# Optimization experiments

Hardware: AMD Instinct MI355X
Metric: run time of the kernel (lower is better)

## Reference

```python
import jax, jax.numpy as jnp
import numpy as np

C, H, W = 512, 192, 192  # feature map dims; 3x3 patches at stride 3 (non-overlapping)


def setup_inputs() -> dict:
    key = jax.random.key(0)
    k1, k2 = jax.random.split(key)
    model_resp = jax.random.normal(k1, (1, C, H, W), dtype=jnp.float32)
    style_resp = jax.random.normal(k2, (1, C, H, W), dtype=jnp.float32)
    return {"model_resp": model_resp, "style_resp": style_resp}


def _unfold3(x):
    # torch.nn.Unfold(kernel=3, stride=3) on (1, C, H, W) -> (C*9, L) after the
    # module's view(patch_count, patch_size) (note: rows are feature channels,
    # columns are spatial locations, matching the original code's dim order).
    _, c, h, w = x.shape
    p = x[0].reshape(c, h // 3, 3, w // 3, 3)          # (c, ph, kh, pw, kw)
    p = p.transpose(0, 2, 4, 1, 3)                      # (c, kh, kw, ph, pw)
    return p.reshape(c * 9, (h // 3) * (w // 3))        # (A, L)


def reference(model_resp, style_resp):
    img = _unfold3(model_resp)                          # (A, L)
    sty = _unfold3(style_resp)                          # (A, L)
    img_norm = 1.0 / jnp.linalg.norm(img, axis=1)       # (A,)
    sty_norm = 1.0 / jnp.linalg.norm(sty, axis=1)       # (A,)
    S = img @ sty.T                                     # (A, A), S[i,j] = img_i . sty_j
    # Faithful to torch: expand(A, A) of a 1-D tensor broadcasts along dim 0,
    # i.e. multiplies COLUMNS by the normalizer vector.
    S1 = S * img_norm[None, :]
    S2 = S1.T * sty_norm[None, :]                       # S2[i,j] = img_norm[i]*sty_norm[j]*(img_j . sty_i)
    nearest = jnp.argmax(S2, axis=0)                    # (A,) int
    max_sim = jnp.max(S2, axis=0)                       # (A,) float (the online-max values)
    return nearest, max_sim
```

## Files before the change

kernel.cpp:

```cpp
#include <hip/hip_runtime.h>
#include <hip/hip_bf16.h>
#include <hip/hip_fp16.h>

#define A_DIM 4608
#define L_DIM 4096
#define CH    512
#define H_DIM 192
#define W_DIM 192

#define BM 128
#define BN 192
#define BK 16
#define NS (L_DIM / BK)

#define CPB 32

typedef _Float16 half8 __attribute__((ext_vector_type(8)));
typedef float   floatx4 __attribute__((ext_vector_type(4)));
typedef float   floatx16 __attribute__((ext_vector_type(16)));

__global__ __launch_bounds__(256) void prep_kernel(
    const float* __restrict__ x0, const float* __restrict__ x1,
    _Float16* __restrict__ Uhi0, _Float16* __restrict__ Ulo0,
    _Float16* __restrict__ Uhi1, _Float16* __restrict__ Ulo1,
    float* __restrict__ ss0, float* __restrict__ ss1) {
  const int which = blockIdx.z;
  const float* __restrict__ x = which ? x1 : x0;
  _Float16* __restrict__ Uhi = which ? Uhi1 : Uhi0;
  _Float16* __restrict__ Ulo = which ? Ulo1 : Ulo0;
  float* __restrict__ ssg = which ? ss1 : ss0;

  const int ph = blockIdx.y;
  const int c0 = blockIdx.x * CPB;
  const int abase = blockIdx.x * (CPB * 9);

  __shared__ _Float16 sHi[CPB * 9 * 8 * 8];
  __shared__ _Float16 sLo[CPB * 9 * 8 * 8];

  const int t = threadIdx.x;

  const int c_l = t >> 3;
  const int s = t & 7;
  const float* __restrict__ rowbase =
      x + ((size_t)(c0 + c_l) * H_DIM + 3 * ph) * W_DIM + s * 24;
  float ssp[9] = {0.f, 0.f, 0.f, 0.f, 0.f, 0.f, 0.f, 0.f, 0.f};

#pragma unroll
  for (int kh = 0; kh < 3; ++kh) {
    const float* __restrict__ rp = rowbase + kh * W_DIM;
    floatx4 v4[6];
#pragma unroll
    for (int i = 0; i < 6; ++i) v4[i] = *(const floatx4*)(rp + i * 4);
    half8 hv[3], lv[3];
#pragma unroll
    for (int i = 0; i < 6; ++i)
#pragma unroll
      for (int j = 0; j < 4; ++j) {
        const int m = i * 4 + j;
        const int kw = m % 3, e = m / 3;
        const float v = v4[i][j];
        ssp[kh * 3 + kw] += v * v;
        const _Float16 h = (_Float16)v;
        hv[kw][e] = h;
        lv[kw][e] = (_Float16)(v - (float)h);
      }
#pragma unroll
    for (int kw = 0; kw < 3; ++kw) {
      const int a_l = c_l * 9 + kh * 3 + kw;
      const int addr = (a_l * 8 + (s ^ (a_l & 7))) * 8;
      *(half8*)&sHi[addr] = hv[kw];
      *(half8*)&sLo[addr] = lv[kw];
    }
  }
#pragma unroll
  for (int q = 0; q < 9; ++q) {
    float v = ssp[q];
    v += __shfl_down(v, 4, 8);
    v += __shfl_down(v, 2, 8);
    v += __shfl_down(v, 1, 8);
    if (s == 0) atomicAdd(&ssg[abase + c_l * 9 + q], v);
  }
  __syncthreads();

#pragma unroll
  for (int i = 0; i < 9; ++i) {
    const int idx = i * 256 + t;
    const int c8 = idx / 288;
    const int a_l = idx - c8 * 288;
    const int addr = (a_l * 8 + (c8 ^ (a_l & 7))) * 8;
    const size_t g = ((size_t)(ph * 8 + c8) * A_DIM + abase + a_l) * 8;
    *(half8*)&Uhi[g] = *(const half8*)&sHi[addr];
    *(half8*)&Ulo[g] = *(const half8*)&sLo[addr];
  }
}

#define GLDS(g, l)                                                          \
  __builtin_amdgcn_global_load_lds(                                        \
      (const __attribute__((address_space(1))) void*)(g),                   \
      (__attribute__((address_space(3))) void*)(l), 16, 0, 0)

#define MFMA_(A, B, C) __builtin_amdgcn_mfma_f32_32x32x16_f16(A, B, C, 0, 0, 0)

__global__ __launch_bounds__(256, 2) void gemm_max_kernel(
    const _Float16* __restrict__ Shi, const _Float16* __restrict__ Slo,
    const _Float16* __restrict__ Ihi, const _Float16* __restrict__ Ilo,
    const float* __restrict__ img_ss,
    unsigned long long* __restrict__ packed) {
  __shared__ _Float16 sm[3 * 10240];

  const int t = threadIdx.x;
  const int lane = t & 63, wv = t >> 6;
  const int wvr = wv >> 1, wvc = wv & 1;
  const int id = blockIdx.x;
  const int g = id / 288, r = id - g * 288;
  const int by = r >> 3, bx = g * 8 + (r & 7);
  const int row0 = by * BM;
  const int col0 = bx * BN;
  const int l31 = lane & 31, hs = lane >> 5;

  floatx16 acc[2][3];
#pragma unroll
  for (int rf = 0; rf < 2; ++rf)
#pragma unroll
    for (int cf = 0; cf < 3; ++cf) acc[rf][cf] = (floatx16)0.f;

  const size_t CH8 = (size_t)A_DIM * 8;

  const size_t aOff = (size_t)(t >> 7) * CH8 + (size_t)(row0 + (t & 127)) * 8;
  const int aDst = t * 8;
  const size_t bG0 =
      (size_t)(t / 192) * CH8 + (size_t)(col0 + (t % 192)) * 8;
  const int bD0 = 4096 + t * 8;
  const int c1 = 256 + t;
  const int mat1 = (c1 >= 384) ? 1 : 0;
  const int rem1 = c1 - mat1 * 384;
  const _Float16* __restrict__ bP1 = mat1 ? Ilo : Ihi;
  const size_t bG1 =
      (size_t)(rem1 / 192) * CH8 + (size_t)(col0 + (rem1 % 192)) * 8;
  const int bD1 = 4096 + mat1 * 3072 + rem1 * 8;
  const int rem2 = 128 + t;
  const size_t bG2 =
      (size_t)(rem2 / 192) * CH8 + (size_t)(col0 + (rem2 % 192)) * 8;
  const int bD2 = 7168 + rem2 * 8;

#define ISSUE(BB, koff)                                  \
  do {                                                   \
    GLDS(Shi + (koff) + aOff, &sm[(BB) + aDst]);         \
    GLDS(Slo + (koff) + aOff, &sm[(BB) + 2048 + aDst]);  \
    GLDS(Ihi + (koff) + bG0, &sm[(BB) + bD0]);           \
    GLDS(bP1 + (koff) + bG1, &sm[(BB) + bD1]);           \
    GLDS(Ilo + (koff) + bG2, &sm[(BB) + bD2]);           \
  } while (0)

  const int aI = (hs * 128 + wvr * 64 + l31) * 8;
  const int bI = (hs * 192 + wvc * 96 + l31) * 8;

  ISSUE(0, 0);
  ISSUE(10240, 2 * CH8);

  int bufC = 0, bufP = 20480;
  for (int ks = 0; ks < NS; ++ks) {
    if (ks < NS - 1) {
      asm volatile("s_waitcnt vmcnt(5)" ::: "memory");
    } else {
      asm volatile("s_waitcnt vmcnt(0)" ::: "memory");
    }
    asm volatile("s_barrier" ::: "memory");

    if (ks + 2 < NS) ISSUE(bufP, (size_t)(ks + 2) * 2 * CH8);

    half8 ah[2], al[2], bh[3], bl[3];
#pragma unroll
    for (int rf = 0; rf < 2; ++rf) {
      ah[rf] = *(const half8*)&sm[bufC + aI + rf * 256];
      al[rf] = *(const half8*)&sm[bufC + 2048 + aI + rf * 256];
    }
#pragma unroll
    for (int cf = 0; cf < 3; ++cf) {
      bh[cf] = *(const half8*)&sm[bufC + 4096 + bI + cf * 256];
      bl[cf] = *(const half8*)&sm[bufC + 7168 + bI + cf * 256];
    }
#pragma unroll
    for (int rf = 0; rf < 2; ++rf)
#pragma unroll
      for (int cf = 0; cf < 3; ++cf)
        acc[rf][cf] = MFMA_(ah[rf], bh[cf], acc[rf][cf]);
#pragma unroll
    for (int rf = 0; rf < 2; ++rf)
#pragma unroll
      for (int cf = 0; cf < 3; ++cf)
        acc[rf][cf] = MFMA_(ah[rf], bl[cf], acc[rf][cf]);
#pragma unroll
    for (int rf = 0; rf < 2; ++rf)
#pragma unroll
      for (int cf = 0; cf < 3; ++cf)
        acc[rf][cf] = MFMA_(al[rf], bh[cf], acc[rf][cf]);

    bufC = (bufC == 20480) ? 0 : bufC + 10240;
    bufP = (bufP == 20480) ? 0 : bufP + 10240;
  }

  float nrv[2][16];
#pragma unroll
  for (int rf = 0; rf < 2; ++rf) {
    const int base_i = row0 + wvr * 64 + rf * 32 + 4 * hs;
#pragma unroll
    for (int g2 = 0; g2 < 4; ++g2) {
      const floatx4 s4 = *(const floatx4*)&img_ss[base_i + 8 * g2];
#pragma unroll
      for (int r2 = 0; r2 < 4; ++r2) nrv[rf][g2 * 4 + r2] = 1.0f / sqrtf(s4[r2]);
    }
  }
#pragma unroll
  for (int cf = 0; cf < 3; ++cf) {
    const int j = col0 + wvc * 96 + cf * 32 + l31;
    float best = -3.4e38f;
    int bi = 0x7FFFFFFF;
#pragma unroll
    for (int rf = 0; rf < 2; ++rf) {
      const int base_i = row0 + wvr * 64 + rf * 32 + 4 * hs;
#pragma unroll
      for (int g2 = 0; g2 < 4; ++g2)
#pragma unroll
        for (int r2 = 0; r2 < 4; ++r2) {
          const int i = base_i + 8 * g2 + r2;
          const float v = acc[rf][cf][g2 * 4 + r2] * nrv[rf][g2 * 4 + r2];
          if (v > best) { best = v; bi = i; }
        }
    }
    const float ov = __shfl_xor(best, 32, 64);
    const int oi = __shfl_xor(bi, 32, 64);
    if (ov > best || (ov == best && oi < bi)) { best = ov; bi = oi; }
    if (hs == 0) {
      const unsigned u = __float_as_uint(best);
      const unsigned key = (u & 0x80000000u) ? ~u : (u | 0x80000000u);
      const unsigned long long pk =
          ((unsigned long long)key << 32) | (unsigned)(~(unsigned)bi);
      atomicMax(&packed[j], pk);
    }
  }
}

__global__ __launch_bounds__(256) void finalize_kernel(
    const unsigned long long* __restrict__ packed,
    const float* __restrict__ sty_ss, float* __restrict__ out) {
  const int j = blockIdx.x * 256 + threadIdx.x;
  if (j >= A_DIM) return;
  const unsigned long long p = packed[j];
  const unsigned key = (unsigned)(p >> 32);
  const unsigned u = (key & 0x80000000u) ? (key ^ 0x80000000u) : ~key;
  const float v = __uint_as_float(u);
  const int idx = (int)(~(unsigned)(p & 0xFFFFFFFFu));
  out[j] = (float)idx;
  out[A_DIM + j] = v * (1.0f / sqrtf(sty_ss[j]));
}

extern "C" void kernel_launch(void* const* d_in, const int* in_sizes, int n_in,
                              void* d_out, int out_size, void* d_ws, size_t ws_size,
                              hipStream_t stream) {
  const float* model = (const float*)d_in[0];
  const float* style = (const float*)d_in[1];
  float* out = (float*)d_out;
  char* ws = (char*)d_ws;

  const size_t usz = (size_t)A_DIM * L_DIM * 2;
  _Float16* img_hi = (_Float16*)(ws);
  _Float16* img_lo = (_Float16*)(ws + usz);
  _Float16* sty_hi = (_Float16*)(ws + 2 * usz);
  _Float16* sty_lo = (_Float16*)(ws + 3 * usz);
  float* img_ss = (float*)(ws + 4 * usz);
  float* sty_ss = img_ss + A_DIM;
  unsigned long long* packed = (unsigned long long*)(img_ss + 2 * A_DIM);

  hipMemsetAsync(img_ss, 0, (size_t)A_DIM * 16, stream);
  prep_kernel<<<dim3(CH / CPB, H_DIM / 3, 2), 256, 0, stream>>>(
      model, style, img_hi, img_lo, sty_hi, sty_lo, img_ss, sty_ss);
  gemm_max_kernel<<<dim3((A_DIM / BM) * (A_DIM / BN)), 256, 0, stream>>>(
      sty_hi, sty_lo, img_hi, img_lo, img_ss, packed);
  finalize_kernel<<<18, 256, 0, stream>>>(packed, sty_ss, out);
}
```

Baseline: 676.6 us.

## Give each wave private LDS buffers to remove block-wide barriers in GEMM loop

```diff
diff --git a/kernel.cpp b/kernel.cpp
--- a/kernel.cpp
+++ b/kernel.cpp
@@ -106,7 +106,7 @@
     const _Float16* __restrict__ Ihi, const _Float16* __restrict__ Ilo,
     const float* __restrict__ img_ss,
     unsigned long long* __restrict__ packed) {
-  __shared__ _Float16 sm[3 * 10240];
+  __shared__ _Float16 sm[4 * 2 * 5120];
 
   const int t = threadIdx.x;
   const int lane = t & 63, wv = t >> 6;
@@ -117,6 +117,7 @@
   const int row0 = by * BM;
   const int col0 = bx * BN;
   const int l31 = lane & 31, hs = lane >> 5;
+  const int wb = wv * 10240;
 
   floatx16 acc[2][3];
 #pragma unroll
@@ -126,78 +127,76 @@
 
   const size_t CH8 = (size_t)A_DIM * 8;
 
-  const size_t aOff = (size_t)(t >> 7) * CH8 + (size_t)(row0 + (t & 127)) * 8;
-  const int aDst = t * 8;
-  const size_t bG0 =
-      (size_t)(t / 192) * CH8 + (size_t)(col0 + (t % 192)) * 8;
-  const int bD0 = 4096 + t * 8;
-  const int c1 = 256 + t;
-  const int mat1 = (c1 >= 384) ? 1 : 0;
-  const int rem1 = c1 - mat1 * 384;
-  const _Float16* __restrict__ bP1 = mat1 ? Ilo : Ihi;
-  const size_t bG1 =
-      (size_t)(rem1 / 192) * CH8 + (size_t)(col0 + (rem1 % 192)) * 8;
-  const int bD1 = 4096 + mat1 * 3072 + rem1 * 8;
-  const int rem2 = 128 + t;
-  const size_t bG2 =
-      (size_t)(rem2 / 192) * CH8 + (size_t)(col0 + (rem2 % 192)) * 8;
-  const int bD2 = 7168 + rem2 * 8;
-
-#define ISSUE(BB, koff)                                  \
-  do {                                                   \
-    GLDS(Shi + (koff) + aOff, &sm[(BB) + aDst]);         \
-    GLDS(Slo + (koff) + aOff, &sm[(BB) + 2048 + aDst]);  \
-    GLDS(Ihi + (koff) + bG0, &sm[(BB) + bD0]);           \
-    GLDS(bP1 + (koff) + bG1, &sm[(BB) + bD1]);           \
-    GLDS(Ilo + (koff) + bG2, &sm[(BB) + bD2]);           \
+  const int rA = row0 + wvr * 64;
+  const int rB = col0 + wvc * 96;
+  const size_t gA0 = (size_t)(rA + lane) * 8;
+  const size_t gA1 = CH8 + gA0;
+  const size_t gB0 = (size_t)(rB + lane) * 8;
+  const size_t gB1 = (lane < 32)
+                         ? (size_t)(rB + 64 + lane) * 8
+                         : CH8 + (size_t)(rB + lane - 32) * 8;
+  const size_t gB2 = CH8 + (size_t)(rB + 32 + lane) * 8;
+  const int dl8 = lane * 8;
+
+#define ISSUE(bb, koff)                                        \
+  do {                                                         \
+    GLDS(Shi + (koff) + gA0, &sm[wb + (bb) + dl8]);            \
+    GLDS(Shi + (koff) + gA1, &sm[wb + (bb) + 512 + dl8]);      \
+    GLDS(Slo + (koff) + gA0, &sm[wb + (bb) + 1024 + dl8]);     \
+    GLDS(Slo + (koff) + gA1, &sm[wb + (bb) + 1536 + dl8]);     \
+    GLDS(Ihi + (koff) + gB0, &sm[wb + (bb) + 2048 + dl8]);     \
+    GLDS(Ihi + (koff) + gB1, &sm[wb + (bb) + 2560 + dl8]);     \
+    GLDS(Ihi + (koff) + gB2, &sm[wb + (bb) + 3072 + dl8]);     \
+    GLDS(Ilo + (koff) + gB0, &sm[wb + (bb) + 3584 + dl8]);     \
+    GLDS(Ilo + (koff) + gB1, &sm[wb + (bb) + 4096 + dl8]);     \
+    GLDS(Ilo + (koff) + gB2, &sm[wb + (bb) + 4608 + dl8]);     \
   } while (0)
 
-  const int aI = (hs * 128 + wvr * 64 + l31) * 8;
-  const int bI = (hs * 192 + wvc * 96 + l31) * 8;
+  const int aI = hs * 512 + l31 * 8;
+  const int bI = hs * 768 + l31 * 8;
+
+#define KSTEP(BOFF, KS)                                                  \
+  do {                                                                   \
+    asm volatile("s_waitcnt lgkmcnt(0)" ::: "memory");                   \
+    if ((KS) + 1 < NS) {                                                 \
+      ISSUE(5120 - (BOFF), (size_t)((KS) + 1) * 2 * CH8);                \
+      asm volatile("s_waitcnt vmcnt(10)" ::: "memory");                  \
+    } else {                                                             \
+      asm volatile("s_waitcnt vmcnt(0)" ::: "memory");                   \
+    }                                                                    \
+    const int base = wb + (BOFF);                                        \
+    half8 ah[2], al[2], bh[3], bl[3];                                    \
+    _Pragma("unroll")                                                    \
+    for (int rf = 0; rf < 2; ++rf) {                                     \
+      ah[rf] = *(const half8*)&sm[base + aI + rf * 256];                 \
+      al[rf] = *(const half8*)&sm[base + 1024 + aI + rf * 256];          \
+    }                                                                    \
+    _Pragma("unroll")                                                    \
+    for (int cf = 0; cf < 3; ++cf) {                                     \
+      bh[cf] = *(const half8*)&sm[base + 2048 + bI + cf * 256];          \
+      bl[cf] = *(const half8*)&sm[base + 3584 + bI + cf * 256];          \
+    }                                                                    \
+    _Pragma("unroll")                                                    \
+    for (int rf = 0; rf < 2; ++rf)                                       \
+      _Pragma("unroll")                                                  \
+      for (int cf = 0; cf < 3; ++cf)                                     \
+        acc[rf][cf] = MFMA_(ah[rf], bh[cf], acc[rf][cf]);                \
+    _Pragma("unroll")                                                    \
+    for (int rf = 0; rf < 2; ++rf)                                       \
+      _Pragma("unroll")                                                  \
+      for (int cf = 0; cf < 3; ++cf)                                     \
+        acc[rf][cf] = MFMA_(ah[rf], bl[cf], acc[rf][cf]);                \
+    _Pragma("unroll")                                                    \
+    for (int rf = 0; rf < 2; ++rf)                                       \
+      _Pragma("unroll")                                                  \
+      for (int cf = 0; cf < 3; ++cf)                                     \
+        acc[rf][cf] = MFMA_(al[rf], bh[cf], acc[rf][cf]);                \
+  } while (0)
 
   ISSUE(0, 0);
-  ISSUE(10240, 2 * CH8);
-
-  int bufC = 0, bufP = 20480;
-  for (int ks = 0; ks < NS; ++ks) {
-    if (ks < NS - 1) {
-      asm volatile("s_waitcnt vmcnt(5)" ::: "memory");
-    } else {
-      asm volatile("s_waitcnt vmcnt(0)" ::: "memory");
-    }
-    asm volatile("s_barrier" ::: "memory");
-
-    if (ks + 2 < NS) ISSUE(bufP, (size_t)(ks + 2) * 2 * CH8);
-
-    half8 ah[2], al[2], bh[3], bl[3];
-#pragma unroll
-    for (int rf = 0; rf < 2; ++rf) {
-      ah[rf] = *(const half8*)&sm[bufC + aI + rf * 256];
-      al[rf] = *(const half8*)&sm[bufC + 2048 + aI + rf * 256];
-    }
-#pragma unroll
-    for (int cf = 0; cf < 3; ++cf) {
-      bh[cf] = *(const half8*)&sm[bufC + 4096 + bI + cf * 256];
-      bl[cf] = *(const half8*)&sm[bufC + 7168 + bI + cf * 256];
-    }
-#pragma unroll
-    for (int rf = 0; rf < 2; ++rf)
-#pragma unroll
-      for (int cf = 0; cf < 3; ++cf)
-        acc[rf][cf] = MFMA_(ah[rf], bh[cf], acc[rf][cf]);
-#pragma unroll
-    for (int rf = 0; rf < 2; ++rf)
-#pragma unroll
-      for (int cf = 0; cf < 3; ++cf)
-        acc[rf][cf] = MFMA_(ah[rf], bl[cf], acc[rf][cf]);
-#pragma unroll
-    for (int rf = 0; rf < 2; ++rf)
-#pragma unroll
-      for (int cf = 0; cf < 3; ++cf)
-        acc[rf][cf] = MFMA_(al[rf], bh[cf], acc[rf][cf]);
-
-    bufC = (bufC == 20480) ? 0 : bufC + 10240;
-    bufP = (bufP == 20480) ? 0 : bufP + 10240;
+  for (int ks = 0; ks < NS; ks += 2) {
+    KSTEP(0, ks);
+    KSTEP(5120, ks + 1);
   }
 
   float nrv[2][16];
```

Measured after the change: 793.8 us. +17.3%, slower.

## Double-buffer LDS with register ping-pong fragments to overlap LDS reads with MFMA

Applied to the files above, without the earlier changes.

```diff
diff --git a/kernel.cpp b/kernel.cpp
--- a/kernel.cpp
+++ b/kernel.cpp
@@ -106,7 +106,7 @@
     const _Float16* __restrict__ Ihi, const _Float16* __restrict__ Ilo,
     const float* __restrict__ img_ss,
     unsigned long long* __restrict__ packed) {
-  __shared__ _Float16 sm[3 * 10240];
+  __shared__ _Float16 sm[2 * 10240];
 
   const int t = threadIdx.x;
   const int lane = t & 63, wv = t >> 6;
@@ -128,8 +128,7 @@
 
   const size_t aOff = (size_t)(t >> 7) * CH8 + (size_t)(row0 + (t & 127)) * 8;
   const int aDst = t * 8;
-  const size_t bG0 =
-      (size_t)(t / 192) * CH8 + (size_t)(col0 + (t % 192)) * 8;
+  const size_t bG0 = (size_t)(t / 192) * CH8 + (size_t)(col0 + (t % 192)) * 8;
   const int bD0 = 4096 + t * 8;
   const int c1 = 256 + t;
   const int mat1 = (c1 >= 384) ? 1 : 0;
@@ -152,52 +151,81 @@
     GLDS(Ilo + (koff) + bG2, &sm[(BB) + bD2]);           \
   } while (0)
 
-  const int aI = (hs * 128 + wvr * 64 + l31) * 8;
-  const int bI = (hs * 192 + wvc * 96 + l31) * 8;
+  const int aI = hs * 1024 + (wvr * 64 + l31) * 8;
+  const int bI = hs * 1536 + (wvc * 96 + l31) * 8;
+
+#define FREAD(AH, AL, BH, BL, BB)                              \
+  do {                                                         \
+    _Pragma("unroll")                                          \
+    for (int rf = 0; rf < 2; ++rf) {                           \
+      AH[rf] = *(const half8*)&sm[(BB) + aI + rf * 256];       \
+      AL[rf] = *(const half8*)&sm[(BB) + 2048 + aI + rf * 256];\
+    }                                                          \
+    _Pragma("unroll")                                          \
+    for (int cf = 0; cf < 3; ++cf) {                           \
+      BH[cf] = *(const half8*)&sm[(BB) + 4096 + bI + cf * 256];\
+      BL[cf] = *(const half8*)&sm[(BB) + 7168 + bI + cf * 256];\
+    }                                                          \
+  } while (0)
+
+#define MM18(AH, AL, BH, BL)                                   \
+  do {                                                         \
+    _Pragma("unroll")                                          \
+    for (int rf = 0; rf < 2; ++rf)                             \
+      _Pragma("unroll")                                        \
+      for (int cf = 0; cf < 3; ++cf)                           \
+        acc[rf][cf] = MFMA_(AH[rf], BH[cf], acc[rf][cf]);      \
+    _Pragma("unroll")                                          \
+    for (int rf = 0; rf < 2; ++rf)                             \
+      _Pragma("unroll")                                        \
+      for (int cf = 0; cf < 3; ++cf)                           \
+        acc[rf][cf] = MFMA_(AH[rf], BL[cf], acc[rf][cf]);      \
+    _Pragma("unroll")                                          \
+    for (int rf = 0; rf < 2; ++rf)                             \
+      _Pragma("unroll")                                        \
+      for (int cf = 0; cf < 3; ++cf)                           \
+        acc[rf][cf] = MFMA_(AL[rf], BH[cf], acc[rf][cf]);      \
+  } while (0)
+
+#define BARRIER asm volatile("s_barrier" ::: "memory")
+#define LGKM0 asm volatile("s_waitcnt lgkmcnt(0)" ::: "memory")
+
+  half8 ahA[2], alA[2], bhA[3], blA[3];
+  half8 ahB[2], alB[2], bhB[3], blB[3];
 
   ISSUE(0, 0);
   ISSUE(10240, 2 * CH8);
-
-  int bufC = 0, bufP = 20480;
-  for (int ks = 0; ks < NS; ++ks) {
-    if (ks < NS - 1) {
+  asm volatile("s_waitcnt vmcnt(5)" ::: "memory");
+  BARRIER;
+  FREAD(ahA, alA, bhA, blA, 0);
+  LGKM0;
+  BARRIER;
+
+  for (int ks = 0; ks < NS; ks += 2) {
+    if (ks + 2 < NS) {
+      ISSUE(0, (size_t)(ks + 2) * 2 * CH8);
       asm volatile("s_waitcnt vmcnt(5)" ::: "memory");
     } else {
       asm volatile("s_waitcnt vmcnt(0)" ::: "memory");
     }
-    asm volatile("s_barrier" ::: "memory");
-
-    if (ks + 2 < NS) ISSUE(bufP, (size_t)(ks + 2) * 2 * CH8);
-
-    half8 ah[2], al[2], bh[3], bl[3];
-#pragma unroll
-    for (int rf = 0; rf < 2; ++rf) {
-      ah[rf] = *(const half8*)&sm[bufC + aI + rf * 256];
-      al[rf] = *(const half8*)&sm[bufC + 2048 + aI + rf * 256];
-    }
-#pragma unroll
-    for (int cf = 0; cf < 3; ++cf) {
-      bh[cf] = *(const half8*)&sm[bufC + 4096 + bI + cf * 256];
-      bl[cf] = *(const half8*)&sm[bufC + 7168 + bI + cf * 256];
-    }
-#pragma unroll
-    for (int rf = 0; rf < 2; ++rf)
-#pragma unroll
-      for (int cf = 0; cf < 3; ++cf)
-        acc[rf][cf] = MFMA_(ah[rf], bh[cf], acc[rf][cf]);
-#pragma unroll
-    for (int rf = 0; rf < 2; ++rf)
-#pragma unroll
-      for (int cf = 0; cf < 3; ++cf)
-        acc[rf][cf] = MFMA_(ah[rf], bl[cf], acc[rf][cf]);
-#pragma unroll
-    for (int rf = 0; rf < 2; ++rf)
-#pragma unroll
-      for (int cf = 0; cf < 3; ++cf)
-        acc[rf][cf] = MFMA_(al[rf], bh[cf], acc[rf][cf]);
-
-    bufC = (bufC == 20480) ? 0 : bufC + 10240;
-    bufP = (bufP == 20480) ? 0 : bufP + 10240;
+    BARRIER;
+    FREAD(ahB, alB, bhB, blB, 10240);
+    MM18(ahA, alA, bhA, blA);
+    LGKM0;
+    BARRIER;
+
+    const bool more = (ks + 2 < NS);
+    if (ks + 3 < NS) {
+      ISSUE(10240, (size_t)(ks + 3) * 2 * CH8);
+      asm volatile("s_waitcnt vmcnt(5)" ::: "memory");
+    } else {
+      asm volatile("s_waitcnt vmcnt(0)" ::: "memory");
+    }
+    BARRIER;
+    if (more) FREAD(ahA, alA, bhA, blA, 0);
+    MM18(ahB, alB, bhB, blB);
+    LGKM0;
+    BARRIER;
   }
 
   float nrv[2][16];
```

Measured after the change: 676.3 us. About the same (-0.0%).
